# Optimization experiments

Hardware: AMD Instinct MI355X
Metric: run time of the kernel (lower is better)

## Reference

```python
import jax, jax.numpy as jnp
import numpy as np

QLEN, KLEN, BSZ, NHEAD, DHEAD = 1024, 1024, 2, 16, 64
RLEN = QLEN + KLEN
SCALE = 1.0 / np.sqrt(DHEAD).astype(np.float32)  # 1/sqrt(d_head)


def setup_inputs() -> dict:
    key = jax.random.key(0)
    ks = jax.random.split(key, 10)
    return {
        "q_head": jax.random.normal(ks[0], (QLEN, BSZ, NHEAD, DHEAD), jnp.float32),
        "k_head_h": jax.random.normal(ks[1], (KLEN, BSZ, NHEAD, DHEAD), jnp.float32),
        "v_head_h": jax.random.normal(ks[2], (KLEN, BSZ, NHEAD, DHEAD), jnp.float32),
        "k_head_r": jax.random.normal(ks[3], (RLEN, BSZ, NHEAD, DHEAD), jnp.float32),
        "seg_embed": jax.random.normal(ks[4], (2, NHEAD, DHEAD), jnp.float32),
        "seg_mat": jax.random.uniform(ks[5], (QLEN, KLEN, BSZ, 2), jnp.float32),
        "r_w_bias": jax.random.normal(ks[6], (NHEAD, DHEAD), jnp.float32),
        "r_r_bias": jax.random.normal(ks[7], (NHEAD, DHEAD), jnp.float32),
        "r_s_bias": jax.random.normal(ks[8], (NHEAD, DHEAD), jnp.float32),
        "attn_mask": jnp.zeros((QLEN, KLEN, 1, 1), jnp.float32),
    }


def _rel_shift(x, klen):
    # x: [qlen, rlen, bsz, n_head] -> [qlen, klen, bsz, n_head]
    x = jnp.transpose(x, (1, 0, 2, 3))[1:]          # drop first position row
    x = jnp.transpose(x, (1, 0, 2, 3))[:, :klen]    # keep first klen columns
    return x


def reference(q_head, k_head_h, v_head_h, k_head_r, seg_embed, seg_mat,
              r_w_bias, r_r_bias, r_s_bias, attn_mask):
    # content-based score
    ac = jnp.einsum('ibnd,jbnd->ijbn', q_head + r_w_bias, k_head_h)
    # position-based score with relative shift
    bd = jnp.einsum('ibnd,jbnd->ijbn', q_head + r_r_bias, k_head_r)
    bd = _rel_shift(bd, klen=ac.shape[1])
    # segment-based score
    ef = jnp.einsum('ibnd,snd->ibns', q_head + r_s_bias, seg_embed)
    ef = jnp.einsum('ijbs,ibns->ijbn', seg_mat, ef)
    attn_score = (ac + bd + ef) * SCALE
    attn_score = attn_score - 1e30 * attn_mask
    attn_prob = jax.nn.softmax(attn_score, axis=1)  # over key dim j
    attn_vec = jnp.einsum('ijbn,jbnd->ibnd', attn_prob, v_head_h)
    return attn_vec
```

## Files before the change

kernel.cpp:

```cpp
#include <hip/hip_runtime.h>

#define QLEN 1024
#define KLEN 1024
#define BSZ 2
#define NHEAD 16
#define DHEAD 64
#define RS 2048
#define BLK_I 64
#define BLK_J 32
#define NT32 (KLEN / BLK_J)
#define NBN (BSZ * NHEAD)

#define SC2f  0.18033688011112440f
#define MBIGf 1.4426950408889634e30f
#define THRf  8.0f

#define SEGP_BYTES  16777216u
#define KT_BYTES    ((size_t)NBN * NT32 * 4096)
#define OPART_BYTES 8388608u
#define ML_BYTES    524288u

typedef __attribute__((ext_vector_type(8))) short s16x8;
typedef __attribute__((ext_vector_type(4))) short s16x4;
typedef __attribute__((ext_vector_type(8))) unsigned short u16x8;
typedef __attribute__((ext_vector_type(4))) unsigned short u16x4;
typedef __attribute__((ext_vector_type(4))) float f32x4;
typedef __attribute__((ext_vector_type(2))) float f32x2;

__device__ __forceinline__ unsigned short f2bf(float f) {
    union { float f; unsigned int u; } x; x.f = f;
    unsigned int r = x.u + 0x7fffu + ((x.u >> 16) & 1u);
    return (unsigned short)(r >> 16);
}
__device__ __forceinline__ float bf2f(unsigned short h) {
    union { unsigned int u; float f; } x; x.u = ((unsigned int)h) << 16;
    return x.f;
}

__device__ __forceinline__ f32x4 mfma16x16x16(s16x4 a, s16x4 b, f32x4 c) {
#if __has_builtin(__builtin_amdgcn_mfma_f32_16x16x16bf16_1k)
    return __builtin_amdgcn_mfma_f32_16x16x16bf16_1k(a, b, c, 0, 0, 0);
#else
    f32x4 d;
    asm("v_mfma_f32_16x16x16_bf16 %0, %1, %2, %3"
        : "=v"(d) : "v"(a), "v"(b), "0"(c));
    return d;
#endif
}

typedef const __attribute__((address_space(1))) unsigned int* gas_t;
typedef __attribute__((address_space(3))) unsigned int* las_t;
__device__ __forceinline__ void gl_lds16(const void* g, void* l) {
    __builtin_amdgcn_global_load_lds((gas_t)g, (las_t)l, 16, 0, 0);
}

__global__ __launch_bounds__(256)
void pack_all_kernel(const float* __restrict__ segmat,
                     const float* __restrict__ mask,
                     const float* __restrict__ kh,
                     const float* __restrict__ kr,
                     const float* __restrict__ v,
                     unsigned short* __restrict__ segT,
                     unsigned short* __restrict__ Kp,
                     unsigned short* __restrict__ Krp,
                     unsigned short* __restrict__ Vtp)
{
    __shared__ float smS[16][32][4];
    __shared__ float smM[16][33];
    __shared__ float VT[32][65];
    const int bid = blockIdx.x;
    const int tid = threadIdx.x;

    if (bid < 2048) {
        const int istrip = bid >> 5;
        const int jt     = bid & 31;
        const int ib     = istrip * 16;
        const int jb     = jt * 32;
        {
            const int il = tid >> 4;
            const int j2 = (tid & 15) * 2;
            const float* sp = segmat + ((size_t)(ib + il) * KLEN + jb + j2) * 4;
            *(f32x4*)&smS[il][j2][0]     = *(const f32x4*)sp;
            *(f32x4*)&smS[il][j2 + 1][0] = *(const f32x4*)(sp + 4);
            const float* mp = mask + (size_t)(ib + il) * KLEN + jb + j2;
            smM[il][j2]     = mp[0] * MBIGf;
            smM[il][j2 + 1] = mp[1] * MBIGf;
        }
        __syncthreads();
        const int k  = tid >> 6;
        const int l  = tid & 63;
        const int q4 = l >> 4;
        const int il = l & 15;
        const int jl = (k >> 1) * 16 + q4 * 4 + (k & 1) * 2;
#pragma unroll
        for (int b = 0; b < 2; ++b) {
            u16x8 o;
#pragma unroll
            for (int e = 0; e < 2; ++e) {
                o[e * 4 + 0] = f2bf(smS[il][jl + e][b * 2]);
                o[e * 4 + 1] = f2bf(smS[il][jl + e][b * 2 + 1]);
                o[e * 4 + 2] = f2bf(smM[il][jl + e]);
                o[e * 4 + 3] = 0;
            }
            unsigned short* op = segT + ((size_t)(b * 64 + istrip) << 16)
                                 + (jt << 11) + tid * 8;
            *(u16x8*)op = o;
        }
    } else {
        const int blk = bid - 2048;
        const int bn  = blk >> 5;
        const int jt  = blk & (NT32 - 1);
        const int b   = bn & 1;
        const int n   = bn >> 1;
        const int boff = b * NHEAD * DHEAD + n * DHEAD;
        const int j0  = jt * BLK_J;

        {
            const int j  = tid >> 3;
            const int dq = (tid & 7) * 8;
            const float* vp = v + (size_t)(j0 + j) * RS + boff + dq;
#pragma unroll
            for (int e = 0; e < 8; ++e) VT[j][dq + e] = vp[e];
        }
        __syncthreads();

        const size_t tb = (size_t)blk * 2048;
        {
            const int row = tid >> 3;
            const int ch  = (tid & 7) ^ (row & 7);
            u16x8 ok, orr;
            const float* hp = kh + (size_t)(j0 + row) * RS + boff + ch * 8;
            const float* rp = kr + (size_t)(j0 + row + 1) * RS + boff + ch * 8;
#pragma unroll
            for (int e = 0; e < 8; ++e) { ok[e] = f2bf(hp[e]); orr[e] = f2bf(rp[e]); }
            *(u16x8*)&Kp [tb + (size_t)tid * 8] = ok;
            *(u16x8*)&Krp[tb + (size_t)tid * 8] = orr;
        }
        {
            const int d  = tid >> 2;
            const int gl = tid & 3;
#pragma unroll
            for (int s = 0; s < 2; ++s) {
                const int gj8 = gl * 2 + s;
                const int ph  = gj8 ^ (d & 7);
                u16x4 ov;
#pragma unroll
                for (int e = 0; e < 4; ++e) ov[e] = f2bf(VT[gj8 * 4 + e][d]);
                *(u16x4*)&Vtp[tb + (size_t)d * 32 + ph * 4] = ov;
            }
        }
    }
}

__global__ __launch_bounds__(256)
void merge_kernel(const unsigned short* __restrict__ opart,
                  const float* __restrict__ ml,
                  float* __restrict__ out)
{
    const int gid = blockIdx.x * 256 + threadIdx.x;
    const int d   = gid & 63;
    const int rr  = gid >> 6;
    const int i   = rr & (QLEN - 1);
    const int n   = (rr >> 10) & (NHEAD - 1);
    const int b   = rr >> 14;
    const int r0  = rr;
    const int r1  = (NBN * QLEN) + rr;
    const float m0 = ml[r0 * 2], l0 = ml[r0 * 2 + 1];
    const float m1 = ml[r1 * 2], l1 = ml[r1 * 2 + 1];
    const float M  = fmaxf(m0, m1);
    const float w0 = __builtin_amdgcn_exp2f(m0 - M);
    const float w1 = __builtin_amdgcn_exp2f(m1 - M);
    const float inv = 1.f / (l0 * w0 + l1 * w1);
    const float o = (bf2f(opart[(size_t)r0 * 64 + d]) * w0
                   + bf2f(opart[(size_t)r1 * 64 + d]) * w1) * inv;
    out[(size_t)i * RS + b * NHEAD * DHEAD + n * DHEAD + d] = o;
}

__global__ __launch_bounds__(256, 4)
void relattn_kernel(const float* __restrict__ q,
                    const float* __restrict__ segemb,
                    const float* __restrict__ rwb,
                    const float* __restrict__ rrb,
                    const float* __restrict__ rsb,
                    const unsigned short* __restrict__ segT,
                    const unsigned short* __restrict__ Kp,
                    const unsigned short* __restrict__ Krp,
                    const unsigned short* __restrict__ Vtp,
                    unsigned short* __restrict__ opart,
                    float* __restrict__ mlpart,
                    float* __restrict__ out,
                    int jsplit, int njt)
{
    __shared__ unsigned short KhL[2][32][64];
    __shared__ unsigned short KrL[2][32][64];
    __shared__ unsigned short VtL[2][64][32];

    const int F = blockIdx.x;
    const int x = F & 7;
    const int k = F >> 3;
    const int g = (k >> 4) * 8 + x;
    const int n = k & 15;
    int i0, b, jsp;
    if (jsplit) { i0 = (g >> 2) * BLK_I; b = (g >> 1) & 1; jsp = g & 1; }
    else        { i0 = (g >> 1) * BLK_I; b = g & 1;        jsp = 0;    }
    const int bn = n * 2 + b;
    const int boff = b * NHEAD * DHEAD + n * DHEAD;

    const int tid  = threadIdx.x;
    const int wave = tid >> 6;
    const int lane = tid & 63;
    const int q4   = lane >> 4;
    const int c    = lane & 15;
    const int iRow = i0 + wave * 16 + c;

    s16x8 qwf[2], qrf[2];
    float e0, e1;
    {
        const float* qp = q + (size_t)iRow * RS + boff;
        float es0 = 0.f, es1 = 0.f;
#pragma unroll
        for (int kk = 0; kk < 2; ++kk) {
            const int off = kk * 32 + q4 * 8;
            const f32x4 q0 = *(const f32x4*)(qp + off);
            const f32x4 q1 = *(const f32x4*)(qp + off + 4);
            const f32x4 w0 = *(const f32x4*)(rwb + n * DHEAD + off);
            const f32x4 w1 = *(const f32x4*)(rwb + n * DHEAD + off + 4);
            const f32x4 r0 = *(const f32x4*)(rrb + n * DHEAD + off);
            const f32x4 r1 = *(const f32x4*)(rrb + n * DHEAD + off + 4);
            const f32x4 sa = *(const f32x4*)(segemb + n * DHEAD + off);
            const f32x4 sb = *(const f32x4*)(segemb + n * DHEAD + off + 4);
            const f32x4 ta = *(const f32x4*)(segemb + (NHEAD + n) * DHEAD + off);
            const f32x4 tb = *(const f32x4*)(segemb + (NHEAD + n) * DHEAD + off + 4);
            const f32x4 ra = *(const f32x4*)(rsb + n * DHEAD + off);
            const f32x4 rb = *(const f32x4*)(rsb + n * DHEAD + off + 4);
            s16x8 tw, tr;
#pragma unroll
            for (int e = 0; e < 4; ++e) {
                tw[e]     = (short)f2bf((q0[e] + w0[e]) * SC2f);
                tw[4 + e] = (short)f2bf((q1[e] + w1[e]) * SC2f);
                tr[e]     = (short)f2bf((q0[e] + r0[e]) * SC2f);
                tr[4 + e] = (short)f2bf((q1[e] + r1[e]) * SC2f);
                es0 += (q0[e] + ra[e]) * sa[e] + (q1[e] + rb[e]) * sb[e];
                es1 += (q0[e] + ra[e]) * ta[e] + (q1[e] + rb[e]) * tb[e];
            }
            qwf[kk] = tw; qrf[kk] = tr;
        }
        es0 += __shfl_xor(es0, 16, 64); es0 += __shfl_xor(es0, 32, 64);
        es1 += __shfl_xor(es1, 16, 64); es1 += __shfl_xor(es1, 32, 64);
        e0 = es0 * SC2f; e1 = es1 * SC2f;
    }

    const int tbase = bn * NT32 + jsp * njt;
    auto stage = [&](int jt, int buf) {
        const size_t toff = ((size_t)(tbase + jt)) << 12;
        const int go = tid * 16;
        const int lo = wave * 1024;
        gl_lds16((const char*)Kp  + toff + go, (char*)&KhL[buf][0][0] + lo);
        gl_lds16((const char*)Krp + toff + go, (char*)&KrL[buf][0][0] + lo);
        gl_lds16((const char*)Vtp + toff + go, (char*)&VtL[buf][0][0] + lo);
    };

    stage(0, 0);
    __syncthreads();

    float m = -INFINITY, lsum = 0.f;
    f32x4 acc[4];
#pragma unroll
    for (int dt = 0; dt < 4; ++dt) acc[dt] = (f32x4)0.f;

    const unsigned short* segW = segT + ((size_t)(b * 64 + (i0 >> 4) + wave) << 16);

    int cur = 0;
    for (int jt = 0; jt < njt; ++jt) {
        if (jt + 1 < njt) stage(jt + 1, cur ^ 1);

        const unsigned short* st = segW + ((jsp * njt + jt) << 11);
        u16x8 pg[4];
        pg[0] = *(const u16x8*)(st + lane * 8);
        pg[1] = *(const u16x8*)(st + 512 + lane * 8);
        pg[2] = *(const u16x8*)(st + 1024 + lane * 8);
        pg[3] = *(const u16x8*)(st + 1536 + lane * 8);

        f32x4 sjT[2];
        sjT[0] = (f32x4)0.f; sjT[1] = (f32x4)0.f;
        __builtin_amdgcn_s_setprio(1);
#pragma unroll
        for (int kk = 0; kk < 2; ++kk)
#pragma unroll
            for (int js = 0; js < 2; ++js) {
                const int row = js * 16 + c;
                const int pcK = ((kk * 4 + q4) ^ (c & 7)) * 8;
                const s16x8 khf = *(const s16x8*)&KhL[cur][row][pcK];
                const s16x8 krf = *(const s16x8*)&KrL[cur][row][pcK];
                sjT[js] = __builtin_amdgcn_mfma_f32_16x16x32_bf16(khf, qwf[kk], sjT[js], 0, 0, 0);
                sjT[js] = __builtin_amdgcn_mfma_f32_16x16x32_bf16(krf, qrf[kk], sjT[js], 0, 0, 0);
            }
        __builtin_amdgcn_s_setprio(0);

        float sc8[8];
#pragma unroll
        for (int js = 0; js < 2; ++js)
#pragma unroll
            for (int r = 0; r < 4; ++r) {
                const u16x8 g2 = pg[js * 2 + (r >> 1)];
                const int bb = (r & 1) * 4;
                sc8[js * 4 + r] = sjT[js][r]
                                  + bf2f(g2[bb]) * e0 + bf2f(g2[bb + 1]) * e1
                                  - bf2f(g2[bb + 2]);
            }
        float pmax = fmaxf(
            fmaxf(fmaxf(sc8[0], sc8[1]), fmaxf(sc8[2], sc8[3])),
            fmaxf(fmaxf(sc8[4], sc8[5]), fmaxf(sc8[6], sc8[7])));

        if (!__all(pmax <= m + THRf)) {
            float mt = pmax;
            mt = fmaxf(mt, __shfl_xor(mt, 16, 64));
            mt = fmaxf(mt, __shfl_xor(mt, 32, 64));
            const float mn  = fmaxf(m, mt);
            const float scl = __builtin_amdgcn_exp2f(m - mn);
            m = mn;
            lsum *= scl;
#pragma unroll
            for (int dt = 0; dt < 4; ++dt) acc[dt] *= scl;
        }

        float p[8], ps = 0.f;
#pragma unroll
        for (int e = 0; e < 8; ++e) {
            p[e] = __builtin_amdgcn_exp2f(sc8[e] - m);
            ps += p[e];
        }
        lsum += ps;

        s16x4 pf4[2];
#pragma unroll
        for (int js = 0; js < 2; ++js) {
            union { unsigned int w[2]; s16x4 v; } pk2;
            asm("v_cvt_pk_bf16_f32 %0, %1, %2" : "=v"(pk2.w[0]) : "v"(p[js*4+0]), "v"(p[js*4+1]));
            asm("v_cvt_pk_bf16_f32 %0, %1, %2" : "=v"(pk2.w[1]) : "v"(p[js*4+2]), "v"(p[js*4+3]));
            pf4[js] = pk2.v;
        }
        __builtin_amdgcn_s_setprio(1);
#pragma unroll
        for (int dt = 0; dt < 4; ++dt) {
            const unsigned short* vrow = &VtL[cur][dt * 16 + c][0];
#pragma unroll
            for (int js = 0; js < 2; ++js) {
                const int ph = (js * 4 + q4) ^ (c & 7);
                const s16x4 vf = *(const s16x4*)(vrow + ph * 4);
                acc[dt] = mfma16x16x16(vf, pf4[js], acc[dt]);
            }
        }
        __builtin_amdgcn_s_setprio(0);

        __syncthreads();
        cur ^= 1;
    }

    lsum += __shfl_xor(lsum, 16, 64);
    lsum += __shfl_xor(lsum, 32, 64);

    if (jsplit) {
        const int rowG = ((jsp * BSZ + b) * NHEAD + n) * QLEN + iRow;
#pragma unroll
        for (int dt = 0; dt < 4; ++dt) {
            u16x4 ob;
#pragma unroll
            for (int e = 0; e < 4; ++e) ob[e] = f2bf(acc[dt][e]);
            *(u16x4*)&opart[(size_t)rowG * 64 + dt * 16 + q4 * 4] = ob;
        }
        if (q4 == 0) {
            mlpart[(size_t)rowG * 2]     = m;
            mlpart[(size_t)rowG * 2 + 1] = lsum;
        }
    } else {
        const float inv = 1.f / lsum;
        float* op = out + (size_t)iRow * RS + boff;
#pragma unroll
        for (int dt = 0; dt < 4; ++dt) {
            const f32x4 o = acc[dt] * inv;
            *(f32x4*)&op[dt * 16 + q4 * 4] = o;
        }
    }
}

extern "C" void kernel_launch(void* const* d_in, const int* in_sizes, int n_in,
                              void* d_out, int out_size, void* d_ws, size_t ws_size,
                              hipStream_t stream) {
    const float* q   = (const float*)d_in[0];
    const float* kh  = (const float*)d_in[1];
    const float* v   = (const float*)d_in[2];
    const float* kr  = (const float*)d_in[3];
    const float* se  = (const float*)d_in[4];
    const float* sm  = (const float*)d_in[5];
    const float* rwb = (const float*)d_in[6];
    const float* rrb = (const float*)d_in[7];
    const float* rsb = (const float*)d_in[8];
    const float* msk = (const float*)d_in[9];
    float* out = (float*)d_out;

    char* wsb = (char*)d_ws;
    unsigned short* segT = (unsigned short*)wsb;
    unsigned short* Kp   = (unsigned short*)(wsb + SEGP_BYTES);
    unsigned short* Krp  = (unsigned short*)(wsb + SEGP_BYTES + KT_BYTES);
    unsigned short* Vtp  = (unsigned short*)(wsb + SEGP_BYTES + 2 * KT_BYTES);
    unsigned short* opart = (unsigned short*)(wsb + SEGP_BYTES + 3 * KT_BYTES);
    float* mlpart = (float*)(wsb + SEGP_BYTES + 3 * KT_BYTES + OPART_BYTES);

    const int jsplit = (ws_size >= (size_t)SEGP_BYTES + 3 * KT_BYTES + OPART_BYTES + ML_BYTES) ? 1 : 0;
    const int njt    = jsplit ? NT32 / 2 : NT32;

    pack_all_kernel<<<2048 + NBN * NT32, 256, 0, stream>>>(sm, msk, kh, kr, v,
                                                           segT, Kp, Krp, Vtp);
    relattn_kernel<<<jsplit ? 1024 : 512, 256, 0, stream>>>(q, se, rwb, rrb, rsb,
                                                            segT, Kp, Krp, Vtp,
                                                            opart, mlpart, out,
                                                            jsplit, njt);
    if (jsplit)
        merge_kernel<<<NBN * QLEN * DHEAD / 256, 256, 0, stream>>>(opart, mlpart, out);
}
```

Before: 57.22 us.

## Generalize key split to four ways and load V fragments directly from global

Generalizes the key-dimension split to 1, 2 or 4 partitions, picked by available workspace, so the main attention kernel launches up to four times as many blocks. The merge kernel becomes a loop over a variable number of partial results. V is now pre-packed in MFMA fragment order, so each wave reads it straight from global memory into registers instead of staging it through LDS. Launch bounds rise to 8 waves per SIMD, which tightens the register budget. The extra split adds more partial-output traffic and a heavier merge step.

```diff
diff --git a/kernel.cpp b/kernel.cpp
--- a/kernel.cpp
+++ b/kernel.cpp
@@ -10,6 +10,7 @@
 #define BLK_J 32
 #define NT32 (KLEN / BLK_J)
 #define NBN (BSZ * NHEAD)
+#define NQ (NBN * QLEN)
 
 #define SC2f  0.18033688011112440f
 #define MBIGf 1.4426950408889634e30f
@@ -17,15 +18,14 @@
 
 #define SEGP_BYTES  16777216u
 #define KT_BYTES    ((size_t)NBN * NT32 * 4096)
-#define OPART_BYTES 8388608u
-#define ML_BYTES    524288u
+#define OPART1_BYTES 4194304u
+#define ML1_BYTES    262144u
 
 typedef __attribute__((ext_vector_type(8))) short s16x8;
 typedef __attribute__((ext_vector_type(4))) short s16x4;
 typedef __attribute__((ext_vector_type(8))) unsigned short u16x8;
 typedef __attribute__((ext_vector_type(4))) unsigned short u16x4;
 typedef __attribute__((ext_vector_type(4))) float f32x4;
-typedef __attribute__((ext_vector_type(2))) float f32x2;
 
 __device__ __forceinline__ unsigned short f2bf(float f) {
     union { float f; unsigned int u; } x; x.f = f;
@@ -137,17 +137,18 @@
             *(u16x8*)&Krp[tb + (size_t)tid * 8] = orr;
         }
         {
-            const int d  = tid >> 2;
-            const int gl = tid & 3;
-#pragma unroll
-            for (int s = 0; s < 2; ++s) {
-                const int gj8 = gl * 2 + s;
-                const int ph  = gj8 ^ (d & 7);
-                u16x4 ov;
-#pragma unroll
-                for (int e = 0; e < 4; ++e) ov[e] = f2bf(VT[gj8 * 4 + e][d]);
-                *(u16x4*)&Vtp[tb + (size_t)d * 32 + ph * 4] = ov;
-            }
+            const int dt = tid >> 6;
+            const int l  = tid & 63;
+            const int q4v = l >> 4;
+            const int cv  = l & 15;
+            const int d   = dt * 16 + cv;
+            u16x8 ov;
+#pragma unroll
+            for (int js = 0; js < 2; ++js)
+#pragma unroll
+                for (int e = 0; e < 4; ++e)
+                    ov[js * 4 + e] = f2bf(VT[js * 16 + q4v * 4 + e][d]);
+            *(u16x8*)&Vtp[tb + (size_t)tid * 8] = ov;
         }
     }
 }
@@ -155,7 +156,7 @@
 __global__ __launch_bounds__(256)
 void merge_kernel(const unsigned short* __restrict__ opart,
                   const float* __restrict__ ml,
-                  float* __restrict__ out)
+                  float* __restrict__ out, int jsp)
 {
     const int gid = blockIdx.x * 256 + threadIdx.x;
     const int d   = gid & 63;
@@ -163,20 +164,19 @@
     const int i   = rr & (QLEN - 1);
     const int n   = (rr >> 10) & (NHEAD - 1);
     const int b   = rr >> 14;
-    const int r0  = rr;
-    const int r1  = (NBN * QLEN) + rr;
-    const float m0 = ml[r0 * 2], l0 = ml[r0 * 2 + 1];
-    const float m1 = ml[r1 * 2], l1 = ml[r1 * 2 + 1];
-    const float M  = fmaxf(m0, m1);
-    const float w0 = __builtin_amdgcn_exp2f(m0 - M);
-    const float w1 = __builtin_amdgcn_exp2f(m1 - M);
-    const float inv = 1.f / (l0 * w0 + l1 * w1);
-    const float o = (bf2f(opart[(size_t)r0 * 64 + d]) * w0
-                   + bf2f(opart[(size_t)r1 * 64 + d]) * w1) * inv;
-    out[(size_t)i * RS + b * NHEAD * DHEAD + n * DHEAD + d] = o;
-}
-
-__global__ __launch_bounds__(256, 4)
+    float M = -INFINITY;
+    for (int p = 0; p < jsp; ++p)
+        M = fmaxf(M, ml[(size_t)(p * NQ + rr) * 2]);
+    float L = 0.f, O = 0.f;
+    for (int p = 0; p < jsp; ++p) {
+        const float w = __builtin_amdgcn_exp2f(ml[(size_t)(p * NQ + rr) * 2] - M);
+        L += ml[(size_t)(p * NQ + rr) * 2 + 1] * w;
+        O += bf2f(opart[(size_t)(p * NQ + rr) * 64 + d]) * w;
+    }
+    out[(size_t)i * RS + b * NHEAD * DHEAD + n * DHEAD + d] = O / L;
+}
+
+__global__ __launch_bounds__(256, 8)
 void relattn_kernel(const float* __restrict__ q,
                     const float* __restrict__ segemb,
                     const float* __restrict__ rwb,
@@ -189,20 +189,21 @@
                     unsigned short* __restrict__ opart,
                     float* __restrict__ mlpart,
                     float* __restrict__ out,
-                    int jsplit, int njt)
+                    int lg, int njt)
 {
     __shared__ unsigned short KhL[2][32][64];
     __shared__ unsigned short KrL[2][32][64];
-    __shared__ unsigned short VtL[2][64][32];
-
+
+    const int jsp = 1 << lg;
     const int F = blockIdx.x;
     const int x = F & 7;
     const int k = F >> 3;
-    const int g = (k >> 4) * 8 + x;
     const int n = k & 15;
-    int i0, b, jsp;
-    if (jsplit) { i0 = (g >> 2) * BLK_I; b = (g >> 1) & 1; jsp = g & 1; }
-    else        { i0 = (g >> 1) * BLK_I; b = g & 1;        jsp = 0;    }
+    const int g = ((k >> 4) << 3) + x;
+    const int jspq = g & (jsp - 1);
+    const int t2 = g >> lg;
+    const int b  = t2 & 1;
+    const int i0 = (t2 >> 1) * BLK_I;
     const int bn = n * 2 + b;
     const int boff = b * NHEAD * DHEAD + n * DHEAD;
 
@@ -250,14 +251,13 @@
         e0 = es0 * SC2f; e1 = es1 * SC2f;
     }
 
-    const int tbase = bn * NT32 + jsp * njt;
+    const int tbase = bn * NT32 + jspq * njt;
     auto stage = [&](int jt, int buf) {
         const size_t toff = ((size_t)(tbase + jt)) << 12;
         const int go = tid * 16;
         const int lo = wave * 1024;
         gl_lds16((const char*)Kp  + toff + go, (char*)&KhL[buf][0][0] + lo);
         gl_lds16((const char*)Krp + toff + go, (char*)&KrL[buf][0][0] + lo);
-        gl_lds16((const char*)Vtp + toff + go, (char*)&VtL[buf][0][0] + lo);
     };
 
     stage(0, 0);
@@ -274,12 +274,18 @@
     for (int jt = 0; jt < njt; ++jt) {
         if (jt + 1 < njt) stage(jt + 1, cur ^ 1);
 
-        const unsigned short* st = segW + ((jsp * njt + jt) << 11);
+        const unsigned short* st = segW + ((jspq * njt + jt) << 11);
         u16x8 pg[4];
         pg[0] = *(const u16x8*)(st + lane * 8);
         pg[1] = *(const u16x8*)(st + 512 + lane * 8);
         pg[2] = *(const u16x8*)(st + 1024 + lane * 8);
         pg[3] = *(const u16x8*)(st + 1536 + lane * 8);
+
+        const unsigned short* vtb = Vtp + (((size_t)(tbase + jt)) << 11);
+        u16x8 vg[4];
+#pragma unroll
+        for (int dt = 0; dt < 4; ++dt)
+            vg[dt] = *(const u16x8*)(vtb + ((dt << 6) + lane) * 8);
 
         f32x4 sjT[2];
         sjT[0] = (f32x4)0.f; sjT[1] = (f32x4)0.f;
@@ -343,13 +349,10 @@
         __builtin_amdgcn_s_setprio(1);
 #pragma unroll
         for (int dt = 0; dt < 4; ++dt) {
-            const unsigned short* vrow = &VtL[cur][dt * 16 + c][0];
-#pragma unroll
-            for (int js = 0; js < 2; ++js) {
-                const int ph = (js * 4 + q4) ^ (c & 7);
-                const s16x4 vf = *(const s16x4*)(vrow + ph * 4);
-                acc[dt] = mfma16x16x16(vf, pf4[js], acc[dt]);
-            }
+            union { u16x8 w; s16x4 h[2]; } vv; vv.w = vg[dt];
+#pragma unroll
+            for (int js = 0; js < 2; ++js)
+                acc[dt] = mfma16x16x16(vv.h[js], pf4[js], acc[dt]);
         }
         __builtin_amdgcn_s_setprio(0);
 
@@ -360,8 +363,8 @@
     lsum += __shfl_xor(lsum, 16, 64);
     lsum += __shfl_xor(lsum, 32, 64);
 
-    if (jsplit) {
-        const int rowG = ((jsp * BSZ + b) * NHEAD + n) * QLEN + iRow;
+    if (lg) {
+        const int rowG = ((jspq * BSZ + b) * NHEAD + n) * QLEN + iRow;
 #pragma unroll
         for (int dt = 0; dt < 4; ++dt) {
             u16x4 ob;
@@ -405,17 +408,20 @@
     unsigned short* Krp  = (unsigned short*)(wsb + SEGP_BYTES + KT_BYTES);
     unsigned short* Vtp  = (unsigned short*)(wsb + SEGP_BYTES + 2 * KT_BYTES);
     unsigned short* opart = (unsigned short*)(wsb + SEGP_BYTES + 3 * KT_BYTES);
-    float* mlpart = (float*)(wsb + SEGP_BYTES + 3 * KT_BYTES + OPART_BYTES);
-
-    const int jsplit = (ws_size >= (size_t)SEGP_BYTES + 3 * KT_BYTES + OPART_BYTES + ML_BYTES) ? 1 : 0;
-    const int njt    = jsplit ? NT32 / 2 : NT32;
+
+    const size_t base = (size_t)SEGP_BYTES + 3 * KT_BYTES;
+    int lg = 0;
+    if (ws_size >= base + 4 * ((size_t)OPART1_BYTES + ML1_BYTES))      lg = 2;
+    else if (ws_size >= base + 2 * ((size_t)OPART1_BYTES + ML1_BYTES)) lg = 1;
+    const int jsp = 1 << lg;
+    const int njt = NT32 >> lg;
+    float* mlpart = (float*)(wsb + base + (size_t)jsp * OPART1_BYTES);
 
     pack_all_kernel<<<2048 + NBN * NT32, 256, 0, stream>>>(sm, msk, kh, kr, v,
                                                            segT, Kp, Krp, Vtp);
-    relattn_kernel<<<jsplit ? 1024 : 512, 256, 0, stream>>>(q, se, rwb, rrb, rsb,
-                                                            segT, Kp, Krp, Vtp,
-                                                            opart, mlpart, out,
-                                                            jsplit, njt);
-    if (jsplit)
-        merge_kernel<<<NBN * QLEN * DHEAD / 256, 256, 0, stream>>>(opart, mlpart, out);
-}
+    relattn_kernel<<<512 * jsp, 256, 0, stream>>>(q, se, rwb, rrb, rsb,
+                                                  segT, Kp, Krp, Vtp,
+                                                  opart, mlpart, out, lg, njt);
+    if (lg)
+        merge_kernel<<<NQ * DHEAD / 256, 256, 0, stream>>>(opart, mlpart, out, jsp);
+}
```

Result: slower. 177.0 us (+209.3%).
